# Optimization experiments

Hardware: AMD Instinct MI355X
Metric: run time of the kernel (lower is better)

The kernel has to match this reference:

```python
import jax, jax.numpy as jnp
import numpy as np

B, C, H, W = 32, 3, 128, 128
HID, NP, P, E, NH = 64, 64, 16, 768, 4
MAX_SCALE = 0.3


def conv3x3(x, w, b):
    y = jax.lax.conv_general_dilated(x, w, (1, 1), 'SAME', dimension_numbers=('NCHW', 'OIHW', 'NCHW'))
    return y + b[None, :, None, None]


def mha(t, qkv_w, qkv_b, out_w, out_b):
    # t: (B, T, E) -> standard multi-head self-attention (eval: no dropout)
    b, T, e = t.shape
    dh = e // NH
    qkv = t @ qkv_w.T + qkv_b
    q, k, v = jnp.split(qkv, 3, axis=-1)
    sh = lambda z: z.reshape(b, T, NH, dh).transpose(0, 2, 1, 3)
    q, k, v = sh(q), sh(k), sh(v)
    a = jax.nn.softmax(jnp.einsum('bhqd,bhkd->bhqk', q, k) * np.float32(1.0 / np.sqrt(dh)), axis=-1)
    o = jnp.einsum('bhqk,bhkd->bhqd', a, v).transpose(0, 2, 1, 3).reshape(b, T, e)
    return o @ out_w.T + out_b


def conv_self_attn(x, in_w, in_b, qkv_w, qkv_b, out_w, out_b, proj_w, proj_b):
    # channels are tokens; project spatial dim H*W -> E, attend, project back
    b, c, h, w = x.shape
    t = x.reshape(b, c, h * w) @ in_w.T + in_b
    t = mha(t, qkv_w, qkv_b, out_w, out_b)
    y = t @ proj_w.T + proj_b
    return y.reshape(b, c, h, w)


def maxpool2(x):
    return jax.lax.reduce_window(x, -jnp.inf, jax.lax.max, (1, 1, 2, 2), (1, 1, 2, 2), 'VALID')


def grid_sample_bilinear(img, gx, gy):
    # img: (B,C,H,W); gx,gy: (B,NP,P,P) normalized coords; align_corners=False, zeros padding
    b, c, h, w = img.shape
    xs = ((gx + 1.0) * w - 1.0) * 0.5
    ys = ((gy + 1.0) * h - 1.0) * 0.5
    x0f = jnp.floor(xs); y0f = jnp.floor(ys)
    wx = xs - x0f; wy = ys - y0f
    x0 = x0f.astype(jnp.int32); x1 = x0 + 1
    y0 = y0f.astype(jnp.int32); y1 = y0 + 1
    flat = img.reshape(b, c, h * w)

    def gather(yi, xi):
        valid = (xi >= 0) & (xi < w) & (yi >= 0) & (yi < h)
        idx = jnp.clip(yi, 0, h - 1) * w + jnp.clip(xi, 0, w - 1)
        vals = jax.vmap(lambda f, i: f[:, i])(flat, idx)  # (B,C,NP,P,P)
        return vals * valid[:, None].astype(img.dtype)

    v00 = gather(y0, x0); v01 = gather(y0, x1)
    v10 = gather(y1, x0); v11 = gather(y1, x1)
    wxb = wx[:, None]; wyb = wy[:, None]  # (B,1,NP,P,P)
    out = (v00 * (1 - wxb) * (1 - wyb) + v01 * wxb * (1 - wyb)
           + v10 * (1 - wxb) * wyb + v11 * wxb * wyb)
    return out.transpose(0, 2, 1, 3, 4).reshape(b * NP, c, P, P)


def setup_inputs() -> dict:
    key = jax.random.key(0)
    ks = jax.random.split(key, 32)
    wgt = lambda k, s: jax.random.normal(k, s, dtype=jnp.float32) * 0.02
    HW1, HW2, HC = H * W, (H // 2) * (W // 2), (H // 2) * (W // 2)
    inp = {}
    inp['x'] = jax.random.normal(ks[0], (B, C, H, W), dtype=jnp.float32)
    inp['conv1_w'] = wgt(ks[1], (HID, C, 3, 3)); inp['conv1_b'] = jnp.zeros((HID,), jnp.float32)
    inp['a1_in_w'] = wgt(ks[2], (E, HW1)); inp['a1_in_b'] = jnp.zeros((E,), jnp.float32)
    inp['a1_qkv_w'] = wgt(ks[3], (3 * E, E)); inp['a1_qkv_b'] = jnp.zeros((3 * E,), jnp.float32)
    inp['a1_out_w'] = wgt(ks[4], (E, E)); inp['a1_out_b'] = jnp.zeros((E,), jnp.float32)
    inp['a1_proj_w'] = wgt(ks[5], (HW1, E)); inp['a1_proj_b'] = jnp.zeros((HW1,), jnp.float32)
    inp['conv2_w'] = wgt(ks[6], (NP, HID, 3, 3)); inp['conv2_b'] = jnp.zeros((NP,), jnp.float32)
    inp['a2_in_w'] = wgt(ks[7], (E, HW2)); inp['a2_in_b'] = jnp.zeros((E,), jnp.float32)
    inp['a2_qkv_w'] = wgt(ks[8], (3 * E, E)); inp['a2_qkv_b'] = jnp.zeros((3 * E,), jnp.float32)
    inp['a2_out_w'] = wgt(ks[9], (E, E)); inp['a2_out_b'] = jnp.zeros((E,), jnp.float32)
    inp['a2_proj_w'] = wgt(ks[10], (HW2, E)); inp['a2_proj_b'] = jnp.zeros((HW2,), jnp.float32)
    inp['fc1_w'] = wgt(ks[11], (HC // 2, HC)); inp['fc1_b'] = jnp.zeros((HC // 2,), jnp.float32)
    inp['fc2_w'] = wgt(ks[12], (4, HC // 2)); inp['fc2_b'] = jnp.zeros((4,), jnp.float32)
    return inp


def reference(x, conv1_w, conv1_b, a1_in_w, a1_in_b, a1_qkv_w, a1_qkv_b, a1_out_w, a1_out_b,
              a1_proj_w, a1_proj_b, conv2_w, conv2_b, a2_in_w, a2_in_b, a2_qkv_w, a2_qkv_b,
              a2_out_w, a2_out_b, a2_proj_w, a2_proj_b, fc1_w, fc1_b, fc2_w, fc2_b):
    b = x.shape[0]
    f = jax.nn.relu(conv3x3(x, conv1_w, conv1_b))
    f = conv_self_attn(f, a1_in_w, a1_in_b, a1_qkv_w, a1_qkv_b, a1_out_w, a1_out_b, a1_proj_w, a1_proj_b)
    f = maxpool2(f)
    f = jax.nn.relu(conv3x3(f, conv2_w, conv2_b))
    f = conv_self_attn(f, a2_in_w, a2_in_b, a2_qkv_w, a2_qkv_b, a2_out_w, a2_out_b, a2_proj_w, a2_proj_b)
    feats = f.reshape(b, NP, -1)
    h1 = jax.nn.relu(feats @ fc1_w.T + fc1_b)
    tp = h1 @ fc2_w.T + fc2_b  # (b, NP, 4)
    translate = jnp.tanh(tp[:, :, :2])
    s = jax.nn.sigmoid(tp[:, :, 2:3]) * MAX_SCALE
    sx = s[:, :, 0]; sy = s[:, :, 0]  # isotropic: repeat
    rot = jnp.tanh(tp[:, :, 3]) * np.float32(np.pi)
    cos = jnp.cos(rot); sin = jnp.sin(rot)
    x_ext = jnp.minimum(sx * jnp.abs(cos) + sy * jnp.abs(sin), 1.0)
    y_ext = jnp.minimum(sx * jnp.abs(sin) + sy * jnp.abs(cos), 1.0)
    translate = translate * (1.0 - jnp.stack([x_ext, y_ext], axis=-1))
    ta = sx * cos; tb_ = -sx * sin; tc = sy * sin; td = sy * cos
    tx = translate[:, :, 0]; ty = translate[:, :, 1]
    base = (2.0 * jnp.arange(P, dtype=jnp.float32) + 1.0) / P - 1.0  # align_corners=False grid
    gx = ta[..., None, None] * base[None, None, None, :] + tb_[..., None, None] * base[None, None, :, None] + tx[..., None, None]
    gy = tc[..., None, None] * base[None, None, None, :] + td[..., None, None] * base[None, None, :, None] + ty[..., None, None]
    patches = grid_sample_bilinear(x, gx, gy)  # (B*NP, C, P, P)
    return (patches, translate)
```

## Files before the change

### kernel.cpp

```cpp
#include <hip/hip_runtime.h>
#include <hip/hip_bf16.h>
#include <math.h>


#define PI_F 3.14159265358979323846f

typedef float f32x4 __attribute__((ext_vector_type(4)));
typedef short short8 __attribute__((ext_vector_type(8)));
typedef unsigned short us4 __attribute__((ext_vector_type(4)));
typedef __hip_bfloat16 bf16;

__device__ __forceinline__ void async16(const void* g, void* l) {
  __builtin_amdgcn_global_load_lds(
      (const __attribute__((address_space(1))) void*)g,
      (__attribute__((address_space(3))) void*)l, 16, 0, 0);
}

template <int MODE>
__global__ __launch_bounds__(256) void gemm_bf16(
    const unsigned short* __restrict__ A, const unsigned short* __restrict__ Bw,
    const float* __restrict__ bias, void* __restrict__ Cout,
    int M, int N, int K, int kchunk) {
  __shared__ unsigned short As[128 * 32];
  __shared__ unsigned short Bs[128 * 32];
  const int tid = threadIdx.x;
  const int bmT = M >> 7, bnT = N >> 7;
  int l = blockIdx.x;
  const int gsize = 8 * bnT;
  int gid = l / gsize;
  int rem = l - gid * gsize;
  int fm = gid * 8;
  int gsz = bmT - fm; if (gsz > 8) gsz = 8;
  const int bm = (fm + rem % gsz) << 7;
  const int bn = (rem / gsz) << 7;
  const int k0 = blockIdx.z * kchunk;
  const int wave = tid >> 6;
  const int lane = tid & 63;
  const int wm = (wave & 1) << 6, wn = (wave >> 1) << 6;
  const int r0 = tid >> 2;
  const int c0 = (tid & 3) << 3;
  const unsigned short* Ag0 = A + (size_t)(bm + r0) * K + k0 + c0;
  const unsigned short* Ag1 = Ag0 + (size_t)64 * K;
  const unsigned short* Bg0 = Bw + (size_t)(bn + r0) * K + k0 + c0;
  const unsigned short* Bg1 = Bg0 + (size_t)64 * K;
  unsigned short* Al = As + wave * 512;
  unsigned short* Bl = Bs + wave * 512;
  f32x4 acc[4][4] = {};
  const int fr = lane & 15;
  const int fk = (lane >> 4) << 3;
  for (int kt = 0; kt < kchunk; kt += 32) {
    async16(Ag0 + kt, Al);
    async16(Ag1 + kt, Al + 2048);
    async16(Bg0 + kt, Bl);
    async16(Bg1 + kt, Bl + 2048);
    __syncthreads();
    short8 af[4], bf[4];
    #pragma unroll
    for (int i = 0; i < 4; ++i)
      af[i] = *(const short8*)(As + ((wm + i * 16 + fr) << 5) + fk);
    #pragma unroll
    for (int i = 0; i < 4; ++i)
      bf[i] = *(const short8*)(Bs + ((wn + i * 16 + fr) << 5) + fk);
    #pragma unroll
    for (int mi = 0; mi < 4; ++mi)
      #pragma unroll
      for (int ni = 0; ni < 4; ++ni)
        acc[mi][ni] = __builtin_amdgcn_mfma_f32_16x16x32_bf16(af[mi], bf[ni], acc[mi][ni], 0, 0, 0);
    __syncthreads();
  }
  const int cr = (lane >> 4) << 2;
  const int cc = lane & 15;
  if (MODE == 0) {
    float* C = (float*)Cout + (size_t)blockIdx.z * M * N;
    #pragma unroll
    for (int mi = 0; mi < 4; ++mi)
      #pragma unroll
      for (int ni = 0; ni < 4; ++ni) {
        int col = bn + wn + ni * 16 + cc;
        #pragma unroll
        for (int r = 0; r < 4; ++r)
          C[(size_t)(bm + wm + mi * 16 + cr + r) * N + col] = acc[mi][ni][r];
      }
  } else {
    #pragma unroll
    for (int ni = 0; ni < 4; ++ni) {
      int col = bn + wn + ni * 16 + cc;
      float bv = bias[col];
      #pragma unroll
      for (int mi = 0; mi < 4; ++mi)
        #pragma unroll
        for (int r = 0; r < 4; ++r) {
          size_t idx = (size_t)(bm + wm + mi * 16 + cr + r) * N + col;
          float v = acc[mi][ni][r] + bv;
          if (MODE == 1) ((float*)Cout)[idx] = v;
          else ((bf16*)Cout)[idx] = __float2bfloat16(v);
        }
    }
  }
}

__global__ __launch_bounds__(256) void reduce_bias_k(
    const float* __restrict__ part, const float* __restrict__ bias,
    bf16* __restrict__ out, int MN, int N, int S, int relu) {
  int i = blockIdx.x * 256 + threadIdx.x;
  if (i >= (MN >> 2)) return;
  float4 s = ((const float4*)part)[i];
  for (int z = 1; z < S; ++z) {
    float4 q = *(const float4*)(part + (size_t)z * MN + i * 4);
    s.x += q.x; s.y += q.y; s.z += q.z; s.w += q.w;
  }
  int nb = (i * 4) % N;
  float4 bv = *(const float4*)(bias + nb);
  s.x += bv.x; s.y += bv.y; s.z += bv.z; s.w += bv.w;
  if (relu) {
    s.x = fmaxf(s.x, 0.f); s.y = fmaxf(s.y, 0.f);
    s.z = fmaxf(s.z, 0.f); s.w = fmaxf(s.w, 0.f);
  }
  bf16 vals[4] = {__float2bfloat16(s.x), __float2bfloat16(s.y),
                  __float2bfloat16(s.z), __float2bfloat16(s.w)};
  *(us4*)(out + (size_t)i * 4) = *(const us4*)vals;
}

__global__ __launch_bounds__(256) void cvt3_k(
    const float* __restrict__ s0, bf16* __restrict__ d0, int n0,
    const float* __restrict__ s1, bf16* __restrict__ d1, int n1,
    const float* __restrict__ s2, bf16* __restrict__ d2, int n2) {
  int i = blockIdx.x * 256 + threadIdx.x;
  const float* s; bf16* d; int j = i;
  if (j < n0) { s = s0; d = d0; }
  else {
    j -= n0;
    if (j < n1) { s = s1; d = d1; }
    else { j -= n1; if (j >= n2) return; s = s2; d = d2; }
  }
  float4 v = ((const float4*)s)[j];
  bf16 vals[4] = {__float2bfloat16(v.x), __float2bfloat16(v.y),
                  __float2bfloat16(v.z), __float2bfloat16(v.w)};
  *(us4*)(d + (size_t)j * 4) = *(const us4*)vals;
}

__global__ __launch_bounds__(256) void cvt_wcl_k(
    const float* __restrict__ w, bf16* __restrict__ wcl) {
  int i = blockIdx.x * 256 + threadIdx.x;
  if (i >= 36864) return;
  int ic = i & 63, oc = (i >> 6) & 63, s = i >> 12;
  wcl[i] = __float2bfloat16(w[oc * 576 + ic * 9 + s]);
}

__global__ __launch_bounds__(256) void conv3x3_relu_c3_fast(
    const float* __restrict__ x, const float* __restrict__ w,
    const float* __restrict__ bias, bf16* __restrict__ out) {
  __shared__ float xs[3][4][132];
  __shared__ float wsm[3][9][64];
  const int tid = threadIdx.x;
  const int b = blockIdx.y;
  const int y0 = blockIdx.x * 2;
  const int xg = (tid & 15) * 8;
  const int row = (tid >> 4) & 1;
  const int oc0 = (tid >> 5) * 8;
  for (int i = tid; i < 3 * 4 * 132; i += 256) {
    int c = i % 132;
    int r = (i / 132) % 4;
    int ic = i / (132 * 4);
    int gy = y0 + r - 1;
    int gx = c - 1;
    float v = 0.f;
    if ((unsigned)gy < 128u && (unsigned)gx < 128u)
      v = x[((size_t)(b * 3 + ic) << 14) + gy * 128 + gx];
    xs[ic][r][c] = v;
  }
  for (int i = tid; i < 3 * 9 * 64; i += 256) {
    int oc = i & 63;
    int k = (i >> 6) % 9;
    int ic = i / (64 * 9);
    wsm[ic][k][oc] = w[oc * 27 + ic * 9 + k];
  }
  __syncthreads();
  float acc[8][8] = {};
  #pragma unroll
  for (int ic = 0; ic < 3; ++ic) {
    #pragma unroll
    for (int ky = 0; ky < 3; ++ky) {
      const float* rp = &xs[ic][row + ky][xg];
      float4 r0 = *(const float4*)(rp);
      float4 r1 = *(const float4*)(rp + 4);
      float4 r2 = *(const float4*)(rp + 8);
      float v[10] = {r0.x, r0.y, r0.z, r0.w, r1.x, r1.y, r1.z, r1.w, r2.x, r2.y};
      #pragma unroll
      for (int kx = 0; kx < 3; ++kx) {
        const float* wr = &wsm[ic][ky * 3 + kx][oc0];
        float4 w0 = *(const float4*)(wr);
        float4 w1 = *(const float4*)(wr + 4);
        float wv[8] = {w0.x, w0.y, w0.z, w0.w, w1.x, w1.y, w1.z, w1.w};
        #pragma unroll
        for (int o = 0; o < 8; ++o)
          #pragma unroll
          for (int p = 0; p < 8; ++p)
            acc[o][p] += wv[o] * v[p + kx];
      }
    }
  }
  #pragma unroll
  for (int o = 0; o < 8; ++o) {
    float bo = bias[oc0 + o];
    bf16 vals[8];
    #pragma unroll
    for (int p = 0; p < 8; ++p) vals[p] = __float2bfloat16(fmaxf(acc[o][p] + bo, 0.f));
    bf16* op = out + ((size_t)(b * 64 + oc0 + o) << 14) + (y0 + row) * 128 + xg;
    *(uint4*)op = *(const uint4*)vals;
  }
}

__global__ __launch_bounds__(256) void maxpool_cl(
    const bf16* __restrict__ y1, bf16* __restrict__ xp) {
  int wave = threadIdx.x >> 6;
  int lane = threadIdx.x & 63;
  int cell = blockIdx.x * 4 + wave;
  int b = blockIdx.y;
  int yp = cell / 66, xq = cell % 66;
  bf16* dst = xp + (((size_t)b * 66 + yp) * 66 + xq) * 64 + lane;
  if (yp == 0 || yp == 65 || xq == 0 || xq == 65) {
    *dst = __float2bfloat16(0.f);
    return;
  }
  int py = yp - 1, px = xq - 1;
  const bf16* sp = y1 + ((size_t)(b * 64 + lane) << 14) + (py * 2) * 128 + px * 2;
  float a = __bfloat162float(sp[0]), bq = __bfloat162float(sp[1]);
  float c = __bfloat162float(sp[128]), d = __bfloat162float(sp[129]);
  *dst = __float2bfloat16(fmaxf(fmaxf(a, bq), fmaxf(c, d)));
}

__global__ __launch_bounds__(256) void conv2_mfma(
    const bf16* __restrict__ xp, const bf16* __restrict__ wcl,
    const float* __restrict__ bias, bf16* __restrict__ f3) {
  __shared__ unsigned short As[128 * 32];
  __shared__ unsigned short Bs[64 * 32];
  const int tid = threadIdx.x;
  const int b = blockIdx.y;
  const int y0 = blockIdx.x * 2;
  const int wave = tid >> 6;
  const int lane = tid & 63;
  const int wm = (wave & 1) << 6;
  const int wn = (wave >> 1) << 5;
  const char* xpB = (const char*)(xp + (size_t)b * 66 * 66 * 64);
  const char* wclB = (const char*)wcl;
  const int sr = tid >> 2;
  const int soff = (tid & 3) << 4;
  unsigned short* Al = As + wave * 512;
  unsigned short* Bl = Bs + wave * 512;
  f32x4 acc[4][2] = {};
  const int fr = lane & 15;
  const int fk = (lane >> 4) << 3;
  for (int tap = 0; tap < 9; ++tap) {
    int dy = tap / 3, dx = tap % 3;
    const char* arow0 = xpB + (((y0 + dy) * 66 + dx) << 7);
    const char* brow = wclB + (tap << 13);
    #pragma unroll
    for (int ch = 0; ch < 2; ++ch) {
      int coff = (ch << 6) + soff;
      async16(arow0 + sr * 128 + coff, Al);
      async16(arow0 + 66 * 128 + sr * 128 + coff, Al + 2048);
      async16(brow + sr * 128 + coff, Bl);
      __syncthreads();
      short8 af[4], bf[2];
      #pragma unroll
      for (int i = 0; i < 4; ++i)
        af[i] = *(const short8*)(As + ((wm + i * 16 + fr) << 5) + fk);
      #pragma unroll
      for (int i = 0; i < 2; ++i)
        bf[i] = *(const short8*)(Bs + ((wn + i * 16 + fr) << 5) + fk);
      #pragma unroll
      for (int mi = 0; mi < 4; ++mi)
        #pragma unroll
        for (int ni = 0; ni < 2; ++ni)
          acc[mi][ni] = __builtin_amdgcn_mfma_f32_16x16x32_bf16(af[mi], bf[ni], acc[mi][ni], 0, 0, 0);
      __syncthreads();
    }
  }
  const int cr = (lane >> 4) << 2;
  const int cc = lane & 15;
  #pragma unroll
  for (int ni = 0; ni < 2; ++ni) {
    int oc = wn + ni * 16 + cc;
    float bv = bias[oc];
    #pragma unroll
    for (int mi = 0; mi < 4; ++mi) {
      int pxb = wm + mi * 16 + cr;
      int y = y0 + (pxb >> 6), xb = pxb & 63;
      bf16 vals[4];
      #pragma unroll
      for (int r = 0; r < 4; ++r)
        vals[r] = __float2bfloat16(fmaxf(acc[mi][ni][r] + bv, 0.f));
      bf16* op = f3 + (((size_t)(b * 64 + oc)) << 12) + y * 64 + xb;
      *(us4*)op = *(const us4*)vals;
    }
  }
}

__global__ __launch_bounds__(64) void attn_scores(
    const float* __restrict__ qkv, float* __restrict__ p, float scale) {
  int tq = blockIdx.x, h = blockIdx.y, b = blockIdx.z;
  int lane = threadIdx.x;
  __shared__ float qrow[192];
  const float* qp = qkv + ((size_t)(b * 64 + tq)) * 2304 + h * 192;
  for (int d = lane; d < 192; d += 64) qrow[d] = qp[d];
  __syncthreads();
  const float* kp = qkv + ((size_t)(b * 64 + lane)) * 2304 + 768 + h * 192;
  float s = 0.f;
  for (int d = 0; d < 192; ++d) s += qrow[d] * kp[d];
  s *= scale;
  float m = s;
  for (int off = 32; off; off >>= 1) m = fmaxf(m, __shfl_xor(m, off));
  float e = expf(s - m);
  float sum = e;
  for (int off = 32; off; off >>= 1) sum += __shfl_xor(sum, off);
  p[(((size_t)b * 4 + h) * 64 + tq) * 64 + lane] = e / sum;
}

__global__ __launch_bounds__(256) void attn_o(
    const float* __restrict__ p, const float* __restrict__ qkv, bf16* __restrict__ o) {
  size_t tid = (size_t)blockIdx.x * 256 + threadIdx.x;
  if (tid >= (size_t)32 * 64 * 768) return;
  int e = (int)(tid % 768);
  int tq = (int)((tid / 768) % 64);
  int b = (int)(tid / (768 * 64));
  int h = e / 192;
  const float* pp = p + (((size_t)b * 4 + h) * 64 + tq) * 64;
  const float* vp = qkv + (size_t)b * 64 * 2304 + 1536 + e;
  float acc = 0.f;
  for (int tk = 0; tk < 64; ++tk) acc += pp[tk] * vp[(size_t)tk * 2304];
  o[tid] = __float2bfloat16(acc);
}

__global__ __launch_bounds__(256) void fc2_wave(
    const bf16* __restrict__ A, const float* __restrict__ Bw,
    const float* __restrict__ bias, float* __restrict__ C, int K) {
  int m = blockIdx.x;
  int n = threadIdx.x >> 6;
  int lane = threadIdx.x & 63;
  const bf16* a = A + (size_t)m * K;
  const float* bb = Bw + (size_t)n * K;
  float acc = 0.f;
  for (int k = lane; k < K; k += 64)
    acc += __bfloat162float(a[k]) * bb[k];
  for (int off = 32; off; off >>= 1) acc += __shfl_xor(acc, off);
  if (lane == 0) C[m * 4 + n] = acc + bias[n];
}

__global__ __launch_bounds__(64) void params_k(
    const float* __restrict__ tp, float* __restrict__ par, float* __restrict__ trans_out) {
  int m = blockIdx.x * 64 + threadIdx.x;
  if (m >= 2048) return;
  float t0 = tp[m * 4 + 0], t1 = tp[m * 4 + 1], t2 = tp[m * 4 + 2], t3 = tp[m * 4 + 3];
  float trx = tanhf(t0), tryy = tanhf(t1);
  float s = (1.f / (1.f + expf(-t2))) * 0.3f;
  float rot = tanhf(t3) * PI_F;
  float c = cosf(rot), sn = sinf(rot);
  float x_ext = fminf(s * fabsf(c) + s * fabsf(sn), 1.f);
  float y_ext = fminf(s * fabsf(sn) + s * fabsf(c), 1.f);
  float tx = trx * (1.f - x_ext);
  float ty = tryy * (1.f - y_ext);
  par[m * 8 + 0] = s * c;
  par[m * 8 + 1] = -s * sn;
  par[m * 8 + 2] = s * sn;
  par[m * 8 + 3] = s * c;
  par[m * 8 + 4] = tx;
  par[m * 8 + 5] = ty;
  trans_out[m * 2 + 0] = tx;
  trans_out[m * 2 + 1] = ty;
}

__global__ __launch_bounds__(256) void sample_k(
    const float* __restrict__ x, const float* __restrict__ par, float* __restrict__ out) {
  int tid = blockIdx.x * 256 + threadIdx.x;
  if (tid >= 32 * 64 * 3 * 256) return;
  int pj = tid & 15, pi = (tid >> 4) & 15;
  int c = (tid >> 8) % 3;
  int bp = tid / 768;
  int b = bp >> 6;
  const float* pp = par + bp * 8;
  float ta = pp[0], tb = pp[1], tc = pp[2], td = pp[3], tx = pp[4], ty = pp[5];
  float bj = (2.f * pj + 1.f) / 16.f - 1.f;
  float bi = (2.f * pi + 1.f) / 16.f - 1.f;
  float gx = ta * bj + tb * bi + tx;
  float gy = tc * bj + td * bi + ty;
  float xs = ((gx + 1.f) * 128.f - 1.f) * 0.5f;
  float ys = ((gy + 1.f) * 128.f - 1.f) * 0.5f;
  float x0f = floorf(xs), y0f = floorf(ys);
  float wx = xs - x0f, wy = ys - y0f;
  int x0 = (int)x0f, y0 = (int)y0f, x1 = x0 + 1, y1 = y0 + 1;
  const float* img = x + ((size_t)b * 3 + c) * 16384;
  auto g = [&](int yi, int xi) -> float {
    bool v = (xi >= 0) && (xi < 128) && (yi >= 0) && (yi < 128);
    int yc = yi < 0 ? 0 : (yi > 127 ? 127 : yi);
    int xc = xi < 0 ? 0 : (xi > 127 ? 127 : xi);
    float val = img[yc * 128 + xc];
    return v ? val : 0.f;
  };
  float v00 = g(y0, x0), v01 = g(y0, x1), v10 = g(y1, x0), v11 = g(y1, x1);
  out[tid] = v00 * (1.f - wx) * (1.f - wy) + v01 * wx * (1.f - wy) +
             v10 * (1.f - wx) * wy + v11 * wx * wy;
}

extern "C" void kernel_launch(void* const* d_in, const int* in_sizes, int n_in,
                              void* d_out, int out_size, void* d_ws, size_t ws_size,
                              hipStream_t stream) {
  const float* x        = (const float*)d_in[0];
  const float* conv1_w  = (const float*)d_in[1];
  const float* conv1_b  = (const float*)d_in[2];
  const float* a1_in_w  = (const float*)d_in[3];
  const float* a1_in_b  = (const float*)d_in[4];
  const float* a1_qkv_w = (const float*)d_in[5];
  const float* a1_qkv_b = (const float*)d_in[6];
  const float* a1_out_w = (const float*)d_in[7];
  const float* a1_out_b = (const float*)d_in[8];
  const float* a1_proj_w = (const float*)d_in[9];
  const float* a1_proj_b = (const float*)d_in[10];
  const float* conv2_w  = (const float*)d_in[11];
  const float* conv2_b  = (const float*)d_in[12];
  const float* a2_in_w  = (const float*)d_in[13];
  const float* a2_in_b  = (const float*)d_in[14];
  const float* a2_qkv_w = (const float*)d_in[15];
  const float* a2_qkv_b = (const float*)d_in[16];
  const float* a2_out_w = (const float*)d_in[17];
  const float* a2_out_b = (const float*)d_in[18];
  const float* a2_proj_w = (const float*)d_in[19];
  const float* a2_proj_b = (const float*)d_in[20];
  const float* fc1_w    = (const float*)d_in[21];
  const float* fc1_b    = (const float*)d_in[22];
  const float* fc2_w    = (const float*)d_in[23];
  const float* fc2_b    = (const float*)d_in[24];
  float* out = (float*)d_out;

  char* ws = (char*)d_ws;
  bf16*  f1   = (bf16*)(ws + 0);
  bf16*  y1   = f1;
  bf16*  f3   = (bf16*)(ws + 0);
  bf16*  h1   = (bf16*)(ws + 33554432);
  float* part = (float*)(ws + 83886080);
  bf16*  xp   = (bf16*)(ws + 83886080);
  bf16*  t    = (bf16*)(ws + 134217728);
  float* qkv  = (float*)(ws + 137363456);
  float* p    = (float*)(ws + 156237824);
  bf16*  o    = (bf16*)(ws + 158334976);
  bf16*  ao   = (bf16*)(ws + 161480704);
  bf16*  y2   = (bf16*)(ws + 164626432);
  float* tp   = (float*)(ws + 181403648);
  float* par  = (float*)(ws + 181436416);
  bf16*  W    = (bf16*)(ws + 181501952);
  bf16*  wcl  = W;
  bf16*  Wq   = (bf16*)(ws + 164626432);
  bf16*  Wo   = (bf16*)(ws + 164626432 + 3538944);

  const unsigned short* Wu = (const unsigned short*)W;
  const unsigned short* Wqu = (const unsigned short*)Wq;
  const unsigned short* Wou = (const unsigned short*)Wo;
  const float scale = 0.07216878364870323f;

  const int n_in1 = 768 * 16384 / 4, n_qkv = 2304 * 768 / 4, n_out = 768 * 768 / 4;
  const int n_in2 = 768 * 4096 / 4;
  const int n_proj1 = 16384 * 768 / 4, n_proj2 = 4096 * 768 / 4, n_fc1 = 2048 * 4096 / 4;

  conv3x3_relu_c3_fast<<<dim3(64, 32), 256, 0, stream>>>(x, conv1_w, conv1_b, f1);
  cvt3_k<<<(n_in1 + n_qkv + n_out + 255) / 256, 256, 0, stream>>>(
      a1_in_w, W, n_in1, a1_qkv_w, Wq, n_qkv, a1_out_w, Wo, n_out);
  gemm_bf16<0><<<dim3(96, 1, 8), 256, 0, stream>>>((const unsigned short*)f1, Wu, nullptr, part, 2048, 768, 16384, 2048);
  reduce_bias_k<<<1536, 256, 0, stream>>>(part, a1_in_b, t, 2048 * 768, 768, 8, 0);
  gemm_bf16<1><<<dim3(288, 1, 1), 256, 0, stream>>>((const unsigned short*)t, Wqu, a1_qkv_b, qkv, 2048, 2304, 768, 768);
  attn_scores<<<dim3(64, 4, 32), 64, 0, stream>>>(qkv, p, scale);
  attn_o<<<6144, 256, 0, stream>>>(p, qkv, o);
  gemm_bf16<0><<<dim3(96, 1, 3), 256, 0, stream>>>((const unsigned short*)o, Wou, nullptr, part, 2048, 768, 768, 256);
  reduce_bias_k<<<1536, 256, 0, stream>>>(part, a1_out_b, ao, 2048 * 768, 768, 3, 0);
  cvt3_k<<<(n_proj1 + 255) / 256, 256, 0, stream>>>(
      a1_proj_w, W, n_proj1, nullptr, nullptr, 0, nullptr, nullptr, 0);
  gemm_bf16<2><<<dim3(2048, 1, 1), 256, 0, stream>>>((const unsigned short*)ao, Wu, a1_proj_b, y1, 2048, 16384, 768, 768);
  cvt_wcl_k<<<144, 256, 0, stream>>>(conv2_w, wcl);
  maxpool_cl<<<dim3(1089, 32), 256, 0, stream>>>(y1, xp);
  conv2_mfma<<<dim3(32, 32), 256, 0, stream>>>(xp, wcl, conv2_b, f3);
  cvt3_k<<<(n_in2 + n_qkv + n_out + 255) / 256, 256, 0, stream>>>(
      a2_in_w, W, n_in2, a2_qkv_w, Wq, n_qkv, a2_out_w, Wo, n_out);
  gemm_bf16<0><<<dim3(96, 1, 4), 256, 0, stream>>>((const unsigned short*)f3, Wu, nullptr, part, 2048, 768, 4096, 1024);
  reduce_bias_k<<<1536, 256, 0, stream>>>(part, a2_in_b, t, 2048 * 768, 768, 4, 0);
  gemm_bf16<1><<<dim3(288, 1, 1), 256, 0, stream>>>((const unsigned short*)t, Wqu, a2_qkv_b, qkv, 2048, 2304, 768, 768);
  attn_scores<<<dim3(64, 4, 32), 64, 0, stream>>>(qkv, p, scale);
  attn_o<<<6144, 256, 0, stream>>>(p, qkv, o);
  gemm_bf16<0><<<dim3(96, 1, 3), 256, 0, stream>>>((const unsigned short*)o, Wou, nullptr, part, 2048, 768, 768, 256);
  reduce_bias_k<<<1536, 256, 0, stream>>>(part, a2_out_b, ao, 2048 * 768, 768, 3, 0);
  cvt3_k<<<(n_proj2 + 255) / 256, 256, 0, stream>>>(
      a2_proj_w, W, n_proj2, nullptr, nullptr, 0, nullptr, nullptr, 0);
  gemm_bf16<2><<<dim3(512, 1, 1), 256, 0, stream>>>((const unsigned short*)ao, Wu, a2_proj_b, y2, 2048, 4096, 768, 768);
  cvt3_k<<<(n_fc1 + 255) / 256, 256, 0, stream>>>(
      fc1_w, W, n_fc1, nullptr, nullptr, 0, nullptr, nullptr, 0);
  gemm_bf16<0><<<dim3(256, 1, 2), 256, 0, stream>>>((const unsigned short*)y2, Wu, nullptr, part, 2048, 2048, 4096, 2048);
  reduce_bias_k<<<4096, 256, 0, stream>>>(part, fc1_b, h1, 2048 * 2048, 2048, 2, 1);
  fc2_wave<<<2048, 256, 0, stream>>>(h1, fc2_w, fc2_b, tp, 2048);
  params_k<<<32, 64, 0, stream>>>(tp, par, out + 1572864);
  sample_k<<<6144, 256, 0, stream>>>(x, par, out);
}
```

Baseline: 902.3 us.

## Fuse attention scores, softmax and PV into one MFMA kernel with bf16 QKV

Replaces the scalar attn_scores and attn_o kernels with one fused kernel per (batch, head). It stages Q, K and transposed V in LDS, computes QK^T and PV with bf16 MFMA, and does the softmax in registers. The QKV GEMM now writes bf16 (mode 2) instead of fp32, which halves that traffic and removes the probability buffer round trip. In exchange, QKV and the probabilities are stored at lower precision, and only 128 blocks are launched.

```diff
diff --git a/kernel.cpp b/kernel.cpp
--- a/kernel.cpp
+++ b/kernel.cpp
@@ -297,39 +297,82 @@
   }
 }
 
-__global__ __launch_bounds__(64) void attn_scores(
-    const float* __restrict__ qkv, float* __restrict__ p, float scale) {
-  int tq = blockIdx.x, h = blockIdx.y, b = blockIdx.z;
-  int lane = threadIdx.x;
-  __shared__ float qrow[192];
-  const float* qp = qkv + ((size_t)(b * 64 + tq)) * 2304 + h * 192;
-  for (int d = lane; d < 192; d += 64) qrow[d] = qp[d];
+__global__ __launch_bounds__(256) void attn_fused(
+    const bf16* __restrict__ qkv, bf16* __restrict__ o, float scale) {
+  __shared__ unsigned short Qs[64][216];
+  __shared__ unsigned short Ks[64][216];
+  __shared__ unsigned short Vt[192][72];
+  __shared__ unsigned short Ps[64][72];
+  const int tid = threadIdx.x;
+  const int b = blockIdx.x >> 2, h = blockIdx.x & 3;
+  const unsigned short* base = (const unsigned short*)qkv + (size_t)b * 64 * 2304 + h * 192;
+  for (int c = tid; c < 1536; c += 256) {
+    int tok = c / 24, idx = (c % 24) * 8;
+    const unsigned short* rp = base + (size_t)tok * 2304 + idx;
+    short8 qv = *(const short8*)(rp);
+    short8 kv = *(const short8*)(rp + 768);
+    short8 vv = *(const short8*)(rp + 1536);
+    *(short8*)&Qs[tok][idx] = qv;
+    *(short8*)&Ks[tok][idx] = kv;
+    #pragma unroll
+    for (int j = 0; j < 8; ++j) Vt[idx + j][tok] = (unsigned short)vv[j];
+  }
   __syncthreads();
-  const float* kp = qkv + ((size_t)(b * 64 + lane)) * 2304 + 768 + h * 192;
-  float s = 0.f;
-  for (int d = 0; d < 192; ++d) s += qrow[d] * kp[d];
-  s *= scale;
-  float m = s;
-  for (int off = 32; off; off >>= 1) m = fmaxf(m, __shfl_xor(m, off));
-  float e = expf(s - m);
-  float sum = e;
-  for (int off = 32; off; off >>= 1) sum += __shfl_xor(sum, off);
-  p[(((size_t)b * 4 + h) * 64 + tq) * 64 + lane] = e / sum;
-}
-
-__global__ __launch_bounds__(256) void attn_o(
-    const float* __restrict__ p, const float* __restrict__ qkv, bf16* __restrict__ o) {
-  size_t tid = (size_t)blockIdx.x * 256 + threadIdx.x;
-  if (tid >= (size_t)32 * 64 * 768) return;
-  int e = (int)(tid % 768);
-  int tq = (int)((tid / 768) % 64);
-  int b = (int)(tid / (768 * 64));
-  int h = e / 192;
-  const float* pp = p + (((size_t)b * 4 + h) * 64 + tq) * 64;
-  const float* vp = qkv + (size_t)b * 64 * 2304 + 1536 + e;
-  float acc = 0.f;
-  for (int tk = 0; tk < 64; ++tk) acc += pp[tk] * vp[(size_t)tk * 2304];
-  o[tid] = __float2bfloat16(acc);
+  const int wave = tid >> 6, lane = tid & 63;
+  const int fr = lane & 15;
+  const int fk = (lane >> 4) << 3;
+  f32x4 accs[4] = {};
+  #pragma unroll
+  for (int kk = 0; kk < 6; ++kk) {
+    short8 aq = *(const short8*)&Qs[wave * 16 + fr][kk * 32 + fk];
+    #pragma unroll
+    for (int n = 0; n < 4; ++n) {
+      short8 bk = *(const short8*)&Ks[n * 16 + fr][kk * 32 + fk];
+      accs[n] = __builtin_amdgcn_mfma_f32_16x16x32_bf16(aq, bk, accs[n], 0, 0, 0);
+    }
+  }
+  const int cr = (lane >> 4) << 2;
+  const int cc = lane & 15;
+  #pragma unroll
+  for (int r = 0; r < 4; ++r) {
+    float v0 = accs[0][r] * scale, v1 = accs[1][r] * scale;
+    float v2 = accs[2][r] * scale, v3 = accs[3][r] * scale;
+    float m = fmaxf(fmaxf(v0, v1), fmaxf(v2, v3));
+    #pragma unroll
+    for (int off = 8; off; off >>= 1) m = fmaxf(m, __shfl_xor(m, off));
+    float e0 = __expf(v0 - m), e1 = __expf(v1 - m);
+    float e2 = __expf(v2 - m), e3 = __expf(v3 - m);
+    float s = e0 + e1 + e2 + e3;
+    #pragma unroll
+    for (int off = 8; off; off >>= 1) s += __shfl_xor(s, off);
+    float inv = 1.f / s;
+    int q = wave * 16 + cr + r;
+    Ps[q][0 * 16 + cc] = __bfloat16_as_ushort(__float2bfloat16(e0 * inv));
+    Ps[q][1 * 16 + cc] = __bfloat16_as_ushort(__float2bfloat16(e1 * inv));
+    Ps[q][2 * 16 + cc] = __bfloat16_as_ushort(__float2bfloat16(e2 * inv));
+    Ps[q][3 * 16 + cc] = __bfloat16_as_ushort(__float2bfloat16(e3 * inv));
+  }
+  __syncthreads();
+  f32x4 acco[12] = {};
+  #pragma unroll
+  for (int kk = 0; kk < 2; ++kk) {
+    short8 ap = *(const short8*)&Ps[wave * 16 + fr][kk * 32 + fk];
+    #pragma unroll
+    for (int j = 0; j < 12; ++j) {
+      short8 bv = *(const short8*)&Vt[j * 16 + fr][kk * 32 + fk];
+      acco[j] = __builtin_amdgcn_mfma_f32_16x16x32_bf16(ap, bv, acco[j], 0, 0, 0);
+    }
+  }
+  bf16* ob = o + (size_t)(b * 64) * 768 + h * 192;
+  #pragma unroll
+  for (int j = 0; j < 12; ++j) {
+    int d = j * 16 + cc;
+    #pragma unroll
+    for (int r = 0; r < 4; ++r) {
+      int q = wave * 16 + cr + r;
+      ob[(size_t)q * 768 + d] = __float2bfloat16(acco[j][r]);
+    }
+  }
 }
 
 __global__ __launch_bounds__(256) void fc2_wave(
@@ -440,8 +483,7 @@
   float* part = (float*)(ws + 83886080);
   bf16*  xp   = (bf16*)(ws + 83886080);
   bf16*  t    = (bf16*)(ws + 134217728);
-  float* qkv  = (float*)(ws + 137363456);
-  float* p    = (float*)(ws + 156237824);
+  bf16*  qkv  = (bf16*)(ws + 137363456);
   bf16*  o    = (bf16*)(ws + 158334976);
   bf16*  ao   = (bf16*)(ws + 161480704);
   bf16*  y2   = (bf16*)(ws + 164626432);
@@ -466,9 +508,8 @@
       a1_in_w, W, n_in1, a1_qkv_w, Wq, n_qkv, a1_out_w, Wo, n_out);
   gemm_bf16<0><<<dim3(96, 1, 8), 256, 0, stream>>>((const unsigned short*)f1, Wu, nullptr, part, 2048, 768, 16384, 2048);
   reduce_bias_k<<<1536, 256, 0, stream>>>(part, a1_in_b, t, 2048 * 768, 768, 8, 0);
-  gemm_bf16<1><<<dim3(288, 1, 1), 256, 0, stream>>>((const unsigned short*)t, Wqu, a1_qkv_b, qkv, 2048, 2304, 768, 768);
-  attn_scores<<<dim3(64, 4, 32), 64, 0, stream>>>(qkv, p, scale);
-  attn_o<<<6144, 256, 0, stream>>>(p, qkv, o);
+  gemm_bf16<2><<<dim3(288, 1, 1), 256, 0, stream>>>((const unsigned short*)t, Wqu, a1_qkv_b, qkv, 2048, 2304, 768, 768);
+  attn_fused<<<128, 256, 0, stream>>>(qkv, o, scale);
   gemm_bf16<0><<<dim3(96, 1, 3), 256, 0, stream>>>((const unsigned short*)o, Wou, nullptr, part, 2048, 768, 768, 256);
   reduce_bias_k<<<1536, 256, 0, stream>>>(part, a1_out_b, ao, 2048 * 768, 768, 3, 0);
   cvt3_k<<<(n_proj1 + 255) / 256, 256, 0, stream>>>(
@@ -481,9 +522,8 @@
       a2_in_w, W, n_in2, a2_qkv_w, Wq, n_qkv, a2_out_w, Wo, n_out);
   gemm_bf16<0><<<dim3(96, 1, 4), 256, 0, stream>>>((const unsigned short*)f3, Wu, nullptr, part, 2048, 768, 4096, 1024);
   reduce_bias_k<<<1536, 256, 0, stream>>>(part, a2_in_b, t, 2048 * 768, 768, 4, 0);
-  gemm_bf16<1><<<dim3(288, 1, 1), 256, 0, stream>>>((const unsigned short*)t, Wqu, a2_qkv_b, qkv, 2048, 2304, 768, 768);
-  attn_scores<<<dim3(64, 4, 32), 64, 0, stream>>>(qkv, p, scale);
-  attn_o<<<6144, 256, 0, stream>>>(p, qkv, o);
+  gemm_bf16<2><<<dim3(288, 1, 1), 256, 0, stream>>>((const unsigned short*)t, Wqu, a2_qkv_b, qkv, 2048, 2304, 768, 768);
+  attn_fused<<<128, 256, 0, stream>>>(qkv, o, scale);
   gemm_bf16<0><<<dim3(96, 1, 3), 256, 0, stream>>>((const unsigned short*)o, Wou, nullptr, part, 2048, 768, 768, 256);
   reduce_bias_k<<<1536, 256, 0, stream>>>(part, a2_out_b, ao, 2048 * 768, 768, 3, 0);
   cvt3_k<<<(n_proj2 + 255) / 256, 256, 0, stream>>>(
```

After: 773.7 us. -14.3%, faster.
